# Performance work log

Hardware: AMD Instinct MI355X
Metric: run time of the kernel (lower is better)

The kernel has to match this reference:

```python
import jax, jax.numpy as jnp
import numpy as np

B, N, D, E = 2, 50000, 128, 640000


def setup_inputs() -> dict:
    key = jax.random.key(0)
    ks = jax.random.split(key, 7)
    x = jax.random.normal(ks[0], (B, N, D), dtype=jnp.float32)
    edge_index = jax.random.randint(ks[1], (2, E), 0, N)
    edge_attr = jax.random.uniform(ks[2], (E,), dtype=jnp.float32)
    s = 1.0 / np.sqrt(D)
    W1 = jax.random.uniform(ks[3], (D, D), jnp.float32, -s, s)
    b1 = jax.random.uniform(ks[4], (D,), jnp.float32, -s, s)
    W2 = jax.random.uniform(ks[5], (D, D), jnp.float32, -s, s)
    b2 = jax.random.uniform(ks[6], (D,), jnp.float32, -s, s)
    return {"x": x, "edge_index": edge_index, "edge_attr": edge_attr,
            "W1": W1, "b1": b1, "W2": W2, "b2": b2}


def _gcn_layer(x, W, b, row, col, norm, n):
    # x: [B, N, D] -> transform then gather-scale-scatter along edges
    h = jnp.einsum('bnd,df->bnf', x, W)
    msg = h[:, row, :] * norm[None, :, None]          # [B, E2, D]
    agg = jax.vmap(lambda m: jax.ops.segment_sum(m, col, num_segments=n))(msg)
    return agg + b


def reference(x, edge_index, edge_attr, W1, b1, W2, b2):
    n = x.shape[1]
    row, col = edge_index[0], edge_index[1]
    # GCNConv default: add self loops (weight 1), symmetric normalization
    loop = jnp.arange(n)
    row2 = jnp.concatenate([row, loop])
    col2 = jnp.concatenate([col, loop])
    w2 = jnp.concatenate([edge_attr, jnp.ones((n,), edge_attr.dtype)])
    deg = jax.ops.segment_sum(w2, col2, num_segments=n)
    dinv = jnp.where(deg > 0, jax.lax.rsqrt(deg), 0.0)
    norm = dinv[row2] * w2 * dinv[col2]               # [E2]
    # dropout is identity in eval mode
    h = jax.nn.relu(_gcn_layer(x, W1, b1, row2, col2, norm, n))
    h = jax.nn.relu(_gcn_layer(h, W2, b2, row2, col2, norm, n))
    return h
```

## Files before the change

kernel.cpp:

```cpp
#include <hip/hip_runtime.h>

#define NNODES 50000
#define NBATCH 2
#define DIM    128
#define NEDGE  640000
#define M_TOT  (NBATCH*NNODES)
#define NXCD   8

typedef unsigned short u16;
typedef unsigned int   u32;
typedef unsigned long long u64;

typedef __attribute__((ext_vector_type(8))) short bf16x8;
typedef __attribute__((ext_vector_type(4))) float f32x4;

__device__ __forceinline__ float bf2f(u16 u){ return __uint_as_float(((u32)u)<<16); }
__device__ __forceinline__ u16 f2bf(float f){
    u32 x = __float_as_uint(f);
    x += 0x7fffu + ((x>>16)&1u);
    return (u16)(x>>16);
}

__global__ __launch_bounds__(256) void count_k(const int* __restrict__ ei,
                                               const float* __restrict__ ea,
                                               u64* __restrict__ part,
                                               u32* __restrict__ rankpack){
    u32 xcc = __builtin_amdgcn_s_getreg(6164) & 7u;
    int e = blockIdx.x*256 + threadIdx.x;
    if (e < NEDGE){
        int c = ei[NEDGE + e];
        u64 inc = (((u64)__float2uint_rn(ea[e] * 16777216.0f)) << 32) | 1ull;
        u64 old = __hip_atomic_fetch_add(&part[(size_t)xcc*NNODES + c], inc,
                                         __ATOMIC_RELAXED, __HIP_MEMORY_SCOPE_WORKGROUP);
        rankpack[e] = ((u32)old & 0xffffu) | (xcc << 16);
    }
}

__global__ __launch_bounds__(256) void scan1(const u64* __restrict__ part,
                                             int* __restrict__ cnt,
                                             int* __restrict__ poff,
                                             float* __restrict__ dinv,
                                             int* colstart, int* bsum){
    __shared__ int s[256];
    int tid = threadIdx.x;
    int n = blockIdx.x*256 + tid;
    int v = 0;
    if (n < NNODES){
        int run = 0; u64 fsum = 0;
        #pragma unroll
        for (int p = 0; p < NXCD; ++p){
            u64 pv = part[(size_t)p*NNODES + n];
            poff[p*NNODES + n] = run;
            run  += (int)(pv & 0xffffffffu);
            fsum += (pv >> 32);
        }
        cnt[n] = run;
        v = run;
        float deg = 1.0f + (float)fsum * (1.0f/16777216.0f);
        dinv[n] = rsqrtf(deg);
    }
    s[tid] = v; __syncthreads();
    #pragma unroll
    for (int off = 1; off < 256; off <<= 1){
        int t = (tid >= off) ? s[tid-off] : 0;
        __syncthreads();
        s[tid] += t;
        __syncthreads();
    }
    if (n < NNODES) colstart[n] = s[tid] - v;
    if (tid == 255) bsum[blockIdx.x] = s[255];
}

__global__ __launch_bounds__(256) void scan2(int* bsum, int nb){
    __shared__ int s[256];
    int tid = threadIdx.x;
    int v = (tid < nb) ? bsum[tid] : 0;
    s[tid] = v; __syncthreads();
    #pragma unroll
    for (int off = 1; off < 256; off <<= 1){
        int t = (tid >= off) ? s[tid-off] : 0;
        __syncthreads();
        s[tid] += t;
        __syncthreads();
    }
    if (tid < nb) bsum[tid] = s[tid] - v;
}

__global__ __launch_bounds__(256) void scan3(int* colstart, const int* bsum){
    int i = blockIdx.x*256 + threadIdx.x;
    if (i < NNODES) colstart[i] += bsum[i >> 8];
}

__global__ __launch_bounds__(256) void fill_k(const int* __restrict__ ei,
                                              const float* __restrict__ ea,
                                              const float* __restrict__ dinv,
                                              const int* __restrict__ colstart,
                                              const int* __restrict__ poff,
                                              const u32* __restrict__ rankpack,
                                              int2* __restrict__ epack){
    int e = blockIdx.x*256 + threadIdx.x;
    if (e < NEDGE){
        int r = ei[e], c = ei[NEDGE + e];
        u32 rp = rankpack[e];
        int pos = colstart[c] + poff[(rp >> 16)*NNODES + c] + (int)(rp & 0xffffu);
        epack[pos] = make_int2(r, __float_as_int(dinv[r] * ea[e] * dinv[c]));
    }
}

__global__ __launch_bounds__(256) void transposeW(const float* __restrict__ W1, u16* __restrict__ Wt1,
                                                  const float* __restrict__ W2, u16* __restrict__ Wt2){
    int i = blockIdx.x*256 + threadIdx.x;
    const float* W = (i < 16384) ? W1 : W2;
    u16* Wt       = (i < 16384) ? Wt1 : Wt2;
    int ii = i & 16383;
    int k = ii >> 7, n = ii & 127;
    Wt[n*DIM + k] = f2bf(W[ii]);
}

__device__ __forceinline__ bf16x8 load_frag(const float* A, size_t off){
    const float4* ap = (const float4*)(A + off);
    float4 lo = ap[0], hi = ap[1];
    bf16x8 r;
    r[0] = (short)f2bf(lo.x); r[1] = (short)f2bf(lo.y);
    r[2] = (short)f2bf(lo.z); r[3] = (short)f2bf(lo.w);
    r[4] = (short)f2bf(hi.x); r[5] = (short)f2bf(hi.y);
    r[6] = (short)f2bf(hi.z); r[7] = (short)f2bf(hi.w);
    return r;
}
__device__ __forceinline__ bf16x8 load_frag(const u16* A, size_t off){
    return *(const bf16x8*)(A + off);
}

template <typename AT>
__global__ __launch_bounds__(256) void gemm128(const AT* __restrict__ A,
                                               const u16* __restrict__ Wt,
                                               u16* __restrict__ H, int M){
    __shared__ u16 Wl[128][136];
    int tid = threadIdx.x;
    {
        const uint4* src = (const uint4*)Wt;
        #pragma unroll
        for (int j = 0; j < 8; ++j){
            int g = tid + j*256;
            int n = g >> 4;
            int k = (g & 15) * 8;
            *(uint4*)&Wl[n][k] = src[g];
        }
    }
    __syncthreads();

    int wave = tid >> 6, lane = tid & 63;
    int quad = lane >> 4, r = lane & 15;
    int row0 = blockIdx.x*256 + wave*64;

    f32x4 acc[4][8];
    #pragma unroll
    for (int mt = 0; mt < 4; ++mt)
        #pragma unroll
        for (int nt = 0; nt < 8; ++nt)
            acc[mt][nt] = (f32x4){0.f,0.f,0.f,0.f};

    #pragma unroll
    for (int ks = 0; ks < 4; ++ks){
        bf16x8 af[4];
        #pragma unroll
        for (int mt = 0; mt < 4; ++mt){
            int row = row0 + mt*16 + r;
            if (row < M)
                af[mt] = load_frag(A, (size_t)row*DIM + ks*32 + quad*8);
            else
                af[mt] = (bf16x8){0,0,0,0,0,0,0,0};
        }
        #pragma unroll
        for (int nt = 0; nt < 8; ++nt){
            bf16x8 bfr = *(const bf16x8*)&Wl[nt*16 + r][ks*32 + quad*8];
            #pragma unroll
            for (int mt = 0; mt < 4; ++mt)
                acc[mt][nt] = __builtin_amdgcn_mfma_f32_16x16x32_bf16(af[mt], bfr, acc[mt][nt], 0, 0, 0);
        }
    }

    #pragma unroll
    for (int mt = 0; mt < 4; ++mt){
        #pragma unroll
        for (int reg = 0; reg < 4; ++reg){
            int row = row0 + mt*16 + quad*4 + reg;
            if (row < M){
                #pragma unroll
                for (int nt = 0; nt < 8; ++nt)
                    H[(size_t)row*DIM + nt*16 + r] = f2bf(acc[mt][nt][reg]);
            }
        }
    }
}

#define EDGE_FMA(W_, V0_, V1_)                                            \
    a0 = fmaf(W_, bf2f((u16)((V0_) & 0xffff)), a0);                       \
    a1 = fmaf(W_, bf2f((u16)((V0_) >> 16)),    a1);                       \
    a2 = fmaf(W_, bf2f((u16)((V1_) & 0xffff)), a2);                       \
    a3 = fmaf(W_, bf2f((u16)((V1_) >> 16)),    a3);

template <bool OUT_F32>
__global__ __launch_bounds__(256) void gather2_k(const u16* __restrict__ H,
                                                 const int2* __restrict__ epack,
                                                 const int* __restrict__ colstart,
                                                 const int* __restrict__ cnt,
                                                 const float* __restrict__ dinv,
                                                 const float* __restrict__ bias,
                                                 void* __restrict__ out){
    int wave = threadIdx.x >> 6, lane = threadIdx.x & 63;
    int n = blockIdx.x*4 + wave;
    if (n >= NNODES) return;
    const u32* H0 = (const u32*)H;
    const u32* H1 = H0 + (size_t)NNODES*64;

    float dn = dinv[n], dn2 = dn*dn;
    u32 sv0 = H0[(size_t)n*64 + lane];
    u32 sv1 = H1[(size_t)n*64 + lane];
    float a0 = dn2*bf2f((u16)(sv0 & 0xffff)), a1 = dn2*bf2f((u16)(sv0 >> 16));
    float a2 = dn2*bf2f((u16)(sv1 & 0xffff)), a3 = dn2*bf2f((u16)(sv1 >> 16));

    int s = colstart[n], c = cnt[n];
    for (int base = 0; base < c; base += 64){
        int m = min(64, c - base);
        int2 ep = make_int2(0, 0);
        if (lane < m) ep = epack[s + base + lane];
        int j = 0;
        for (; j + 4 <= m; j += 4){
            int   r0 = __shfl(ep.x, j+0), r1 = __shfl(ep.x, j+1);
            int   r2 = __shfl(ep.x, j+2), r3 = __shfl(ep.x, j+3);
            float w0 = __int_as_float(__shfl(ep.y, j+0));
            float w1 = __int_as_float(__shfl(ep.y, j+1));
            float w2 = __int_as_float(__shfl(ep.y, j+2));
            float w3 = __int_as_float(__shfl(ep.y, j+3));
            u32 v00 = H0[(size_t)r0*64 + lane], v10 = H1[(size_t)r0*64 + lane];
            u32 v01 = H0[(size_t)r1*64 + lane], v11 = H1[(size_t)r1*64 + lane];
            u32 v02 = H0[(size_t)r2*64 + lane], v12 = H1[(size_t)r2*64 + lane];
            u32 v03 = H0[(size_t)r3*64 + lane], v13 = H1[(size_t)r3*64 + lane];
            EDGE_FMA(w0, v00, v10)
            EDGE_FMA(w1, v01, v11)
            EDGE_FMA(w2, v02, v12)
            EDGE_FMA(w3, v03, v13)
        }
        for (; j < m; ++j){
            int   rr = __shfl(ep.x, j);
            float ww = __int_as_float(__shfl(ep.y, j));
            u32 v0 = H0[(size_t)rr*64 + lane], v1 = H1[(size_t)rr*64 + lane];
            EDGE_FMA(ww, v0, v1)
        }
    }
    float bb0 = bias[lane*2], bb1 = bias[lane*2 + 1];
    a0 = fmaxf(a0 + bb0, 0.f); a1 = fmaxf(a1 + bb1, 0.f);
    a2 = fmaxf(a2 + bb0, 0.f); a3 = fmaxf(a3 + bb1, 0.f);
    if (OUT_F32){
        float2* O = (float2*)out;
        O[(size_t)n*64 + lane]            = make_float2(a0, a1);
        O[(size_t)(NNODES + n)*64 + lane] = make_float2(a2, a3);
    } else {
        u32* O = (u32*)out;
        O[(size_t)n*64 + lane]            = (u32)f2bf(a0) | ((u32)f2bf(a1) << 16);
        O[(size_t)(NNODES + n)*64 + lane] = (u32)f2bf(a2) | ((u32)f2bf(a3) << 16);
    }
}

extern "C" void kernel_launch(void* const* d_in, const int* in_sizes, int n_in,
                              void* d_out, int out_size, void* d_ws, size_t ws_size,
                              hipStream_t stream){
    const float* x  = (const float*)d_in[0];
    const int*   ei = (const int*)  d_in[1];
    const float* ea = (const float*)d_in[2];
    const float* W1 = (const float*)d_in[3];
    const float* b1 = (const float*)d_in[4];
    const float* W2 = (const float*)d_in[5];
    const float* b2 = (const float*)d_in[6];

    char* p = (char*)d_ws;
    auto alloc = [&](size_t bytes)->char*{ char* r = p; p += (bytes + 511) & ~(size_t)511; return r; };
    u64*   part     = (u64*)  alloc((size_t)NXCD*NNODES*8);
    u32*   rankpack = (u32*)  alloc((size_t)NEDGE*4);
    int*   poff     = (int*)  alloc((size_t)NXCD*NNODES*4);
    float* dinv     = (float*)alloc(NNODES*4);
    int*   cnt      = (int*)  alloc(NNODES*4);
    int*   colstart = (int*)  alloc(NNODES*4);
    int*   bsum     = (int*)  alloc(1024);
    int2*  epack    = (int2*) alloc((size_t)NEDGE*8);
    u16*   Wt1      = (u16*)  alloc(DIM*DIM*2);
    u16*   Wt2      = (u16*)  alloc(DIM*DIM*2);
    u16*   h        = (u16*)  alloc((size_t)M_TOT*DIM*2);
    u16*   o1       = (u16*)  alloc((size_t)M_TOT*DIM*2);

    const int NBL_N = (NNODES + 255)/256;
    const int NBL_E = (NEDGE  + 255)/256;
    const int NTILE = (M_TOT + 255)/256;
    const int NBL_G = (NNODES + 3)/4;

    hipMemsetAsync(part, 0, (size_t)NXCD*NNODES*8, stream);
    transposeW<<<128, 256, 0, stream>>>(W1, Wt1, W2, Wt2);
    count_k<<<NBL_E, 256, 0, stream>>>(ei, ea, part, rankpack);
    scan1  <<<NBL_N, 256, 0, stream>>>(part, cnt, poff, dinv, colstart, bsum);
    scan2  <<<1,     256, 0, stream>>>(bsum, NBL_N);
    scan3  <<<NBL_N, 256, 0, stream>>>(colstart, bsum);
    fill_k <<<NBL_E, 256, 0, stream>>>(ei, ea, dinv, colstart, poff, rankpack, epack);

    gemm128<float><<<NTILE, 256, 0, stream>>>(x, Wt1, h, M_TOT);
    gather2_k<false><<<NBL_G, 256, 0, stream>>>(h, epack, colstart, cnt, dinv, b1, o1);
    gemm128<u16>  <<<NTILE, 256, 0, stream>>>(o1, Wt2, h, M_TOT);
    gather2_k<true> <<<NBL_G, 256, 0, stream>>>(h, epack, colstart, cnt, dinv, b2, d_out);
}
```

Baseline: 286.3 us.

## Split gather by batch across blocks, unroll 8 edges, fuse scan kernels

The neighbour-gather kernel now gives each batch its own block, with batches interleaved in block index, instead of one wave handling both batches. Each wave loads one u32 per edge and processes 8 edges per iteration; padding lanes carry weight zero, so no tail loop is needed. The aim is more waves in flight and more independent loads per wave to hide gather latency. The cost is that the edge list and index metadata are read twice, once per batch. The second and third scan kernels are merged, so each block redundantly scans the block sums and applies its own offset, which saves one launch.

```diff
diff --git a/kernel.cpp b/kernel.cpp
--- a/kernel.cpp
+++ b/kernel.cpp
@@ -6,6 +6,7 @@
 #define NEDGE  640000
 #define M_TOT  (NBATCH*NNODES)
 #define NXCD   8
+#define NBL_N  196
 
 typedef unsigned short u16;
 typedef unsigned int   u32;
@@ -71,10 +72,10 @@
     if (tid == 255) bsum[blockIdx.x] = s[255];
 }
 
-__global__ __launch_bounds__(256) void scan2(int* bsum, int nb){
+__global__ __launch_bounds__(256) void scan23(int* colstart, const int* __restrict__ bsum){
     __shared__ int s[256];
     int tid = threadIdx.x;
-    int v = (tid < nb) ? bsum[tid] : 0;
+    int v = (tid < NBL_N) ? bsum[tid] : 0;
     s[tid] = v; __syncthreads();
     #pragma unroll
     for (int off = 1; off < 256; off <<= 1){
@@ -83,12 +84,9 @@
         s[tid] += t;
         __syncthreads();
     }
-    if (tid < nb) bsum[tid] = s[tid] - v;
-}
-
-__global__ __launch_bounds__(256) void scan3(int* colstart, const int* bsum){
-    int i = blockIdx.x*256 + threadIdx.x;
-    if (i < NNODES) colstart[i] += bsum[i >> 8];
+    int add = s[blockIdx.x] - bsum[blockIdx.x];
+    int i = blockIdx.x*256 + tid;
+    if (i < NNODES) colstart[i] += add;
 }
 
 __global__ __launch_bounds__(256) void fill_k(const int* __restrict__ ei,
@@ -194,72 +192,68 @@
     }
 }
 
-#define EDGE_FMA(W_, V0_, V1_)                                            \
-    a0 = fmaf(W_, bf2f((u16)((V0_) & 0xffff)), a0);                       \
-    a1 = fmaf(W_, bf2f((u16)((V0_) >> 16)),    a1);                       \
-    a2 = fmaf(W_, bf2f((u16)((V1_) & 0xffff)), a2);                       \
-    a3 = fmaf(W_, bf2f((u16)((V1_) >> 16)),    a3);
+#define EFMA(W_, V_)                                        \
+    a0 = fmaf(W_, bf2f((u16)((V_) & 0xffff)), a0);          \
+    a1 = fmaf(W_, bf2f((u16)((V_) >> 16)),    a1);
 
 template <bool OUT_F32>
-__global__ __launch_bounds__(256) void gather2_k(const u16* __restrict__ H,
-                                                 const int2* __restrict__ epack,
-                                                 const int* __restrict__ colstart,
-                                                 const int* __restrict__ cnt,
-                                                 const float* __restrict__ dinv,
-                                                 const float* __restrict__ bias,
-                                                 void* __restrict__ out){
+__global__ __launch_bounds__(256) void gather1b_k(const u16* __restrict__ H,
+                                                  const int2* __restrict__ epack,
+                                                  const int* __restrict__ colstart,
+                                                  const int* __restrict__ cnt,
+                                                  const float* __restrict__ dinv,
+                                                  const float* __restrict__ bias,
+                                                  void* __restrict__ out){
     int wave = threadIdx.x >> 6, lane = threadIdx.x & 63;
-    int n = blockIdx.x*4 + wave;
+    int bid = blockIdx.x;
+    int batch = bid & 1;
+    int n = (bid >> 1)*4 + wave;
     if (n >= NNODES) return;
-    const u32* H0 = (const u32*)H;
-    const u32* H1 = H0 + (size_t)NNODES*64;
+    const u32* Hb = (const u32*)H + (size_t)batch*NNODES*64;
 
     float dn = dinv[n], dn2 = dn*dn;
-    u32 sv0 = H0[(size_t)n*64 + lane];
-    u32 sv1 = H1[(size_t)n*64 + lane];
-    float a0 = dn2*bf2f((u16)(sv0 & 0xffff)), a1 = dn2*bf2f((u16)(sv0 >> 16));
-    float a2 = dn2*bf2f((u16)(sv1 & 0xffff)), a3 = dn2*bf2f((u16)(sv1 >> 16));
+    u32 sv = Hb[(size_t)n*64 + lane];
+    float a0 = dn2*bf2f((u16)(sv & 0xffff));
+    float a1 = dn2*bf2f((u16)(sv >> 16));
 
     int s = colstart[n], c = cnt[n];
     for (int base = 0; base < c; base += 64){
         int m = min(64, c - base);
         int2 ep = make_int2(0, 0);
         if (lane < m) ep = epack[s + base + lane];
-        int j = 0;
-        for (; j + 4 <= m; j += 4){
-            int   r0 = __shfl(ep.x, j+0), r1 = __shfl(ep.x, j+1);
-            int   r2 = __shfl(ep.x, j+2), r3 = __shfl(ep.x, j+3);
+        for (int j = 0; j < m; j += 8){
+            int r0 = __shfl(ep.x, j+0), r1 = __shfl(ep.x, j+1);
+            int r2 = __shfl(ep.x, j+2), r3 = __shfl(ep.x, j+3);
+            int r4 = __shfl(ep.x, j+4), r5 = __shfl(ep.x, j+5);
+            int r6 = __shfl(ep.x, j+6), r7 = __shfl(ep.x, j+7);
             float w0 = __int_as_float(__shfl(ep.y, j+0));
             float w1 = __int_as_float(__shfl(ep.y, j+1));
             float w2 = __int_as_float(__shfl(ep.y, j+2));
             float w3 = __int_as_float(__shfl(ep.y, j+3));
-            u32 v00 = H0[(size_t)r0*64 + lane], v10 = H1[(size_t)r0*64 + lane];
-            u32 v01 = H0[(size_t)r1*64 + lane], v11 = H1[(size_t)r1*64 + lane];
-            u32 v02 = H0[(size_t)r2*64 + lane], v12 = H1[(size_t)r2*64 + lane];
-            u32 v03 = H0[(size_t)r3*64 + lane], v13 = H1[(size_t)r3*64 + lane];
-            EDGE_FMA(w0, v00, v10)
-            EDGE_FMA(w1, v01, v11)
-            EDGE_FMA(w2, v02, v12)
-            EDGE_FMA(w3, v03, v13)
-        }
-        for (; j < m; ++j){
-            int   rr = __shfl(ep.x, j);
-            float ww = __int_as_float(__shfl(ep.y, j));
-            u32 v0 = H0[(size_t)rr*64 + lane], v1 = H1[(size_t)rr*64 + lane];
-            EDGE_FMA(ww, v0, v1)
-        }
-    }
-    float bb0 = bias[lane*2], bb1 = bias[lane*2 + 1];
-    a0 = fmaxf(a0 + bb0, 0.f); a1 = fmaxf(a1 + bb1, 0.f);
-    a2 = fmaxf(a2 + bb0, 0.f); a3 = fmaxf(a3 + bb1, 0.f);
+            float w4 = __int_as_float(__shfl(ep.y, j+4));
+            float w5 = __int_as_float(__shfl(ep.y, j+5));
+            float w6 = __int_as_float(__shfl(ep.y, j+6));
+            float w7 = __int_as_float(__shfl(ep.y, j+7));
+            u32 v0 = Hb[(size_t)r0*64 + lane];
+            u32 v1 = Hb[(size_t)r1*64 + lane];
+            u32 v2 = Hb[(size_t)r2*64 + lane];
+            u32 v3 = Hb[(size_t)r3*64 + lane];
+            u32 v4 = Hb[(size_t)r4*64 + lane];
+            u32 v5 = Hb[(size_t)r5*64 + lane];
+            u32 v6 = Hb[(size_t)r6*64 + lane];
+            u32 v7 = Hb[(size_t)r7*64 + lane];
+            EFMA(w0, v0) EFMA(w1, v1) EFMA(w2, v2) EFMA(w3, v3)
+            EFMA(w4, v4) EFMA(w5, v5) EFMA(w6, v6) EFMA(w7, v7)
+        }
+    }
+    a0 = fmaxf(a0 + bias[lane*2    ], 0.f);
+    a1 = fmaxf(a1 + bias[lane*2 + 1], 0.f);
     if (OUT_F32){
         float2* O = (float2*)out;
-        O[(size_t)n*64 + lane]            = make_float2(a0, a1);
-        O[(size_t)(NNODES + n)*64 + lane] = make_float2(a2, a3);
+        O[(size_t)(batch*NNODES + n)*64 + lane] = make_float2(a0, a1);
     } else {
         u32* O = (u32*)out;
-        O[(size_t)n*64 + lane]            = (u32)f2bf(a0) | ((u32)f2bf(a1) << 16);
-        O[(size_t)(NNODES + n)*64 + lane] = (u32)f2bf(a2) | ((u32)f2bf(a3) << 16);
+        O[(size_t)(batch*NNODES + n)*64 + lane] = (u32)f2bf(a0) | ((u32)f2bf(a1) << 16);
     }
 }
 
@@ -289,21 +283,19 @@
     u16*   h        = (u16*)  alloc((size_t)M_TOT*DIM*2);
     u16*   o1       = (u16*)  alloc((size_t)M_TOT*DIM*2);
 
-    const int NBL_N = (NNODES + 255)/256;
     const int NBL_E = (NEDGE  + 255)/256;
     const int NTILE = (M_TOT + 255)/256;
-    const int NBL_G = (NNODES + 3)/4;
+    const int NBL_G = 2*((NNODES + 3)/4);
 
     hipMemsetAsync(part, 0, (size_t)NXCD*NNODES*8, stream);
     transposeW<<<128, 256, 0, stream>>>(W1, Wt1, W2, Wt2);
     count_k<<<NBL_E, 256, 0, stream>>>(ei, ea, part, rankpack);
     scan1  <<<NBL_N, 256, 0, stream>>>(part, cnt, poff, dinv, colstart, bsum);
-    scan2  <<<1,     256, 0, stream>>>(bsum, NBL_N);
-    scan3  <<<NBL_N, 256, 0, stream>>>(colstart, bsum);
+    scan23 <<<NBL_N, 256, 0, stream>>>(colstart, bsum);
     fill_k <<<NBL_E, 256, 0, stream>>>(ei, ea, dinv, colstart, poff, rankpack, epack);
 
     gemm128<float><<<NTILE, 256, 0, stream>>>(x, Wt1, h, M_TOT);
-    gather2_k<false><<<NBL_G, 256, 0, stream>>>(h, epack, colstart, cnt, dinv, b1, o1);
+    gather1b_k<false><<<NBL_G, 256, 0, stream>>>(h, epack, colstart, cnt, dinv, b1, o1);
     gemm128<u16>  <<<NTILE, 256, 0, stream>>>(o1, Wt2, h, M_TOT);
-    gather2_k<true> <<<NBL_G, 256, 0, stream>>>(h, epack, colstart, cnt, dinv, b2, d_out);
-}
+    gather1b_k<true> <<<NBL_G, 256, 0, stream>>>(h, epack, colstart, cnt, dinv, b2, d_out);
+}
```

Result: no change. 285.1 us (-0.4%).
